# Kernel tuning notes

Hardware: AMD Instinct MI355X
Metric: run time of the kernel (lower is better)

The kernel has to match this reference:

```python
import jax, jax.numpy as jnp
import numpy as np

B, E, C, N, NNZ = 64, 100000, 80000, 10000, 1600000
EPS = 1e-5  # GroupLayerNorm eps


def setup_inputs() -> dict:
    key = jax.random.key(0)
    ks = jax.random.split(key, 8)
    x = jax.random.normal(ks[0], (B, E), dtype=jnp.float32)
    # sparse layer nonzero coordinates (graph-structure-constrained weights)
    w_in_rows = jax.random.randint(ks[1], (NNZ,), 0, E)    # edge index (input dim)
    w_in_cols = jax.random.randint(ks[2], (NNZ,), 0, C)    # hidden channel index
    w_out_rows = jax.random.randint(ks[3], (NNZ,), 0, C)   # hidden channel index
    w_out_cols = jax.random.randint(ks[4], (NNZ,), 0, E)   # edge index (output dim)
    # xavier-like scale: avg fan_in per hidden channel ~ NNZ/C
    scale_in = np.sqrt(2.0 / (NNZ / C + NNZ / E)).astype(np.float32)
    v_in = jax.random.normal(ks[5], (NNZ,), dtype=jnp.float32) * scale_in
    v_out = jax.random.normal(ks[6], (NNZ,), dtype=jnp.float32) * scale_in
    b_in = jnp.zeros((C,), jnp.float32)
    b_out = jnp.zeros((E,), jnp.float32)
    gamma = jnp.ones((C,), jnp.float32)   # GroupLayerNorm affine scale (per channel)
    beta = jnp.zeros((C,), jnp.float32)   # GroupLayerNorm affine shift
    channel_groups = jnp.arange(C, dtype=jnp.int64) // (C // N)  # 8 channels per node
    return {
        'x': x, 'v_in': v_in, 'b_in': b_in, 'v_out': v_out, 'b_out': b_out,
        'gamma': gamma, 'beta': beta,
        'w_in_rows': w_in_rows, 'w_in_cols': w_in_cols,
        'w_out_rows': w_out_rows, 'w_out_cols': w_out_cols,
        'channel_groups': channel_groups,
    }


def _sparse_linear(x, rows, cols, values, bias, out_dim):
    # out[b, c] = sum_{k: cols[k]==c} x[b, rows[k]] * values[k] + bias[c]
    contrib = x[:, rows] * values  # [B, nnz]
    out = jnp.zeros((x.shape[0], out_dim), x.dtype).at[:, cols].add(contrib)
    return out + bias


def _group_layer_norm(h, groups, gamma, beta):
    # per-node-group layernorm over that node's channels
    Bsz = h.shape[0]
    counts = jnp.zeros((N,), h.dtype).at[groups].add(1.0)
    gsum = jnp.zeros((Bsz, N), h.dtype).at[:, groups].add(h)
    gsq = jnp.zeros((Bsz, N), h.dtype).at[:, groups].add(h * h)
    mean = gsum / counts
    var = gsq / counts - mean * mean
    hn = (h - mean[:, groups]) * jax.lax.rsqrt(var[:, groups] + EPS)
    return gamma * hn + beta


def reference(x, v_in, b_in, v_out, b_out, gamma, beta,
              w_in_rows, w_in_cols, w_out_rows, w_out_cols, channel_groups):
    # 1. input sparse linear: edges -> hidden channels
    h = _sparse_linear(x, w_in_rows, w_in_cols, v_in, b_in, C)
    # 2. norm_first=True: GroupLayerNorm then nonlinearity (ELU)
    h = _group_layer_norm(h, channel_groups, gamma, beta)
    h = jax.nn.elu(h)
    # 3. output sparse linear: hidden channels -> edges
    out = _sparse_linear(h, w_out_rows, w_out_cols, v_out, b_out, E)
    # 4. dropout p=0 (identity), residual
    return out + x
```

## Files before the change

### kernel.cpp

```cpp
#include <hip/hip_runtime.h>
#include <hip/hip_bf16.h>

#define B_   64
#define E_   100000
#define C_   80000
#define N_   10000
#define GS   8
#define NNZ_ 1600000
#define EPS_ 1e-5f

#define SHIFT 7
#define BK    128
#define NBLK  256
#define CHUNK (NNZ_ / NBLK)
#define NBMAX 800
#define SCAN_CHUNK 1024
#define SORTT 512
#define PT    1024
#define NTT   782
#define BSCAP 3072

__global__ __launch_bounds__(SORTT) void prep_kernel(
        const float* __restrict__ x, __hip_bfloat16* __restrict__ xT,
        const int* __restrict__ cols1, int* __restrict__ blkcnt1, int nb1,
        const int* __restrict__ cols2, int* __restrict__ blkcnt2, int nb2) {
    __shared__ int hist[NBMAX];
    __shared__ float tile[2][64][65];
    const int b = blockIdx.x;
    const int t = threadIdx.x;
    if (b < 2 * NBLK) {
        const bool p2 = b >= NBLK;
        const int* __restrict__ cols = p2 ? cols2 : cols1;
        int* __restrict__ blkcnt     = p2 ? blkcnt2 : blkcnt1;
        const int nb  = p2 ? nb2 : nb1;
        const int blk = p2 ? (b - NBLK) : b;
        for (int j = t; j < nb; j += SORTT) hist[j] = 0;
        __syncthreads();
        const int base = blk * CHUNK;
        const int end  = min(NNZ_, base + CHUNK);
        for (int k = base + t; k < end; k += SORTT)
            atomicAdd(&hist[cols[k] >> SHIFT], 1);
        __syncthreads();
        for (int j = t; j < nb; j += SORTT) blkcnt[j * NBLK + blk] = hist[j];
    } else {
        const int tb  = b - 2 * NBLK;
        const int sub = t >> 8;
        const int tt  = t & 255;
        const int c   = tt & 63;
        const int r4  = tt >> 6;
        const int e0  = tb * 128 + sub * 64;
#pragma unroll
        for (int j = 0; j < 16; ++j) {
            int br = r4 * 16 + j;
            int e  = e0 + c;
            if (e < E_) tile[sub][c][br] = x[br * E_ + e];
        }
        __syncthreads();
#pragma unroll
        for (int j = 0; j < 16; ++j) {
            int er = r4 * 16 + j;
            int e  = e0 + er;
            if (e < E_) xT[e * 64 + c] = __float2bfloat16(tile[sub][er][c]);
        }
    }
}

__global__ void scan_partial_kernel(const int* __restrict__ c1, int* __restrict__ p1,
                                    int dim1, int np1,
                                    const int* __restrict__ c2, int* __restrict__ p2,
                                    int dim2) {
    __shared__ int red[256];
    const bool ph2 = (int)blockIdx.x >= np1;
    const int* __restrict__ counts = ph2 ? c2 : c1;
    int* __restrict__ partials     = ph2 ? p2 : p1;
    const int dim = ph2 ? dim2 : dim1;
    const int cb  = ph2 ? (blockIdx.x - np1) : blockIdx.x;
    const int t    = threadIdx.x;
    const int base = cb * SCAN_CHUNK + t * 4;
    int s = 0;
#pragma unroll
    for (int j = 0; j < 4; ++j) { int i = base + j; if (i < dim) s += counts[i]; }
    red[t] = s;
    __syncthreads();
    for (int d = 128; d > 0; d >>= 1) {
        if (t < d) red[t] += red[t + d];
        __syncthreads();
    }
    if (t == 0) partials[cb] = red[0];
}

__global__ void scan_base_kernel(int* __restrict__ p1, int np1,
                                 int* __restrict__ p2, int np2) {
    __shared__ int buf[256];
    int* __restrict__ partials = blockIdx.x ? p2 : p1;
    const int nparts           = blockIdx.x ? np2 : np1;
    const int t = threadIdx.x;
    buf[t] = (t < nparts) ? partials[t] : 0;
    __syncthreads();
    for (int d = 1; d < 256; d <<= 1) {
        int v = (t >= d) ? buf[t - d] : 0;
        __syncthreads();
        buf[t] += v;
        __syncthreads();
    }
    if (t < nparts) partials[t] = (t == 0) ? 0 : buf[t - 1];
}

__global__ void scan_emit_kernel(const int* __restrict__ c1, const int* __restrict__ p1,
                                 int* __restrict__ b1, int dim1, int np1,
                                 const int* __restrict__ c2, const int* __restrict__ p2,
                                 int* __restrict__ b2, int dim2) {
    __shared__ int red[256];
    const bool ph2 = (int)blockIdx.x >= np1;
    const int* __restrict__ counts   = ph2 ? c2 : c1;
    const int* __restrict__ partials = ph2 ? p2 : p1;
    int* __restrict__ bases          = ph2 ? b2 : b1;
    const int dim = ph2 ? dim2 : dim1;
    const int cb  = ph2 ? (blockIdx.x - np1) : blockIdx.x;
    const int t    = threadIdx.x;
    const int base = cb * SCAN_CHUNK + t * 4;
    int v[4];
    int s = 0;
#pragma unroll
    for (int j = 0; j < 4; ++j) {
        int i = base + j;
        v[j] = (i < dim) ? counts[i] : 0;
        s += v[j];
    }
    red[t] = s;
    __syncthreads();
    for (int d = 1; d < 256; d <<= 1) {
        int u = (t >= d) ? red[t - d] : 0;
        __syncthreads();
        red[t] += u;
        __syncthreads();
    }
    int run = partials[cb] + ((t == 0) ? 0 : red[t - 1]);
#pragma unroll
    for (int j = 0; j < 4; ++j) {
        int i = base + j;
        if (i < dim) bases[i] = run;
        run += v[j];
    }
}

__global__ __launch_bounds__(PT) void place_kernel(const int* __restrict__ rows,
                             const int* __restrict__ cols,
                             const float* __restrict__ vals, const int* __restrict__ bases,
                             uint2* __restrict__ binned, int nb) {
    __shared__ uint2 staged[CHUNK];
    __shared__ unsigned short bof[CHUNK];
    __shared__ int hist[NBMAX];
    __shared__ int cur[NBMAX];
    __shared__ int goff[NBMAX];
    __shared__ int red[PT];
    const int t    = threadIdx.x;
    const int blk  = blockIdx.x;
    const int base = blk * CHUNK;
    const int n    = min(NNZ_, base + CHUNK) - base;
    for (int j = t; j < nb; j += PT) hist[j] = 0;
    __syncthreads();
    for (int k = t; k < n; k += PT) atomicAdd(&hist[cols[base + k] >> SHIFT], 1);
    __syncthreads();
    int lv[2];
    int s = 0;
    const int b0 = t * 2;
#pragma unroll
    for (int j = 0; j < 2; ++j) {
        int idx = b0 + j;
        lv[j] = (idx < nb) ? hist[idx] : 0;
        s += lv[j];
    }
    red[t] = s;
    __syncthreads();
    for (int d = 1; d < PT; d <<= 1) {
        int v = (t >= d) ? red[t - d] : 0;
        __syncthreads();
        red[t] += v;
        __syncthreads();
    }
    int run = (t == 0) ? 0 : red[t - 1];
#pragma unroll
    for (int j = 0; j < 2; ++j) {
        int idx = b0 + j;
        if (idx < nb) {
            cur[idx]  = run;
            goff[idx] = bases[idx * NBLK + blk] - run;
        }
        run += lv[j];
    }
    __syncthreads();
    for (int k = t; k < n; k += PT) {
        const int c = cols[base + k];
        const int j = c >> SHIFT;
        const int p = atomicAdd(&cur[j], 1);
        staged[p] = make_uint2((unsigned)rows[base + k] | ((unsigned)(c & (BK - 1)) << 17),
                               __float_as_uint(vals[base + k]));
        bof[p] = (unsigned short)j;
    }
    __syncthreads();
    for (int k = t; k < n; k += PT) {
        const int j = bof[k];
        binned[goff[j] + k] = staged[k];
    }
}

__global__ __launch_bounds__(PT) void binsort_kernel(const uint2* __restrict__ binned,
                               const int* __restrict__ bases,
                               int* __restrict__ offsets, float2* __restrict__ csr,
                               int nb, int dim) {
    __shared__ int hist[BK];
    __shared__ int sc[BK];
    __shared__ int cur[BK];
    __shared__ float2 stage[BSCAP];
    const int t   = threadIdx.x;
    const int bkt = blockIdx.x;
    if (t < BK) hist[t] = 0;
    __syncthreads();
    const int beg = bases[bkt * NBLK];
    const int end = (bkt + 1 < nb) ? bases[(bkt + 1) * NBLK] : NNZ_;
    const int cnt = end - beg;
    for (int i = beg + t; i < end; i += PT)
        atomicAdd(&hist[binned[i].x >> 17], 1);
    __syncthreads();
    if (t < BK) sc[t] = hist[t];
    __syncthreads();
    for (int d = 1; d < BK; d <<= 1) {
        int v = (t < BK && t >= d) ? sc[t - d] : 0;
        __syncthreads();
        if (t < BK) sc[t] += v;
        __syncthreads();
    }
    const bool inlds = (cnt <= BSCAP);
    if (t < BK) {
        const int exl = (t == 0) ? 0 : sc[t - 1];
        cur[t] = inlds ? exl : beg + exl;
        const int c = bkt * BK + t;
        if (c < dim) offsets[c] = beg + exl;
    }
    if (t == 0 && bkt == nb - 1) offsets[dim] = NNZ_;
    __syncthreads();
    if (inlds) {
        for (int i = beg + t; i < end; i += PT) {
            const uint2 e = binned[i];
            const int pos = atomicAdd(&cur[e.x >> 17], 1);
            stage[pos] = make_float2(__int_as_float((int)(e.x & 0x1FFFFu)),
                                     __uint_as_float(e.y));
        }
        __syncthreads();
        for (int k = t; k < cnt; k += PT) csr[beg + k] = stage[k];
    } else {
        for (int i = beg + t; i < end; i += PT) {
            const uint2 e = binned[i];
            const int pos = atomicAdd(&cur[e.x >> 17], 1);
            csr[pos] = make_float2(__int_as_float((int)(e.x & 0x1FFFFu)),
                                   __uint_as_float(e.y));
        }
    }
}

__device__ __forceinline__ float col_dot(const float2* __restrict__ csr,
                                         const __hip_bfloat16* __restrict__ src,
                                         int beg, int end, int lane, float a0i) {
    float a[16];
    a[0] = a0i;
#pragma unroll
    for (int j = 1; j < 16; ++j) a[j] = 0.f;
    const __hip_bfloat16* __restrict__ srcl = src + lane;
    int i = beg;
#define USTEP(J)                                                                \
    {                                                                           \
        const float2 eJ = csr[i + (J)];                                         \
        const int    rJ = __float_as_int(eJ.x);                                 \
        a[J] = fmaf(eJ.y, __bfloat162float(srcl[rJ * 64]), a[J]);               \
    }
    for (; i + 16 <= end; i += 16) {
        USTEP(0)  USTEP(1)  USTEP(2)  USTEP(3)
        USTEP(4)  USTEP(5)  USTEP(6)  USTEP(7)
        USTEP(8)  USTEP(9)  USTEP(10) USTEP(11)
        USTEP(12) USTEP(13) USTEP(14) USTEP(15)
    }
    for (; i + 4 <= end; i += 4) {
        USTEP(0) USTEP(1) USTEP(2) USTEP(3)
    }
    for (; i < end; ++i) {
        USTEP(0)
    }
#undef USTEP
    const float s01 = (a[0] + a[1]) + (a[2] + a[3]);
    const float s23 = (a[4] + a[5]) + (a[6] + a[7]);
    const float s45 = (a[8] + a[9]) + (a[10] + a[11]);
    const float s67 = (a[12] + a[13]) + (a[14] + a[15]);
    return (s01 + s23) + (s45 + s67);
}

__global__ __launch_bounds__(256, 8) void gather_kernel(
        const float2* __restrict__ csr, const int* __restrict__ offsets,
        const __hip_bfloat16* __restrict__ src, const float* __restrict__ bias,
        __hip_bfloat16* __restrict__ dst, int dim) {
    const int wave = (blockIdx.x * blockDim.x + threadIdx.x) >> 6;
    const int lane = threadIdx.x & 63;
    if (wave >= dim) return;
    const int beg = __builtin_amdgcn_readfirstlane(offsets[wave]);
    const int end = __builtin_amdgcn_readfirstlane(offsets[wave + 1]);
    dst[wave * 64 + lane] = __float2bfloat16(
        col_dot(csr, src, beg, end, lane, bias ? bias[wave] : 0.f));
}

__global__ void gln_elu_kernel(__hip_bfloat16* __restrict__ h,
                               const float* __restrict__ gamma, const float* __restrict__ beta) {
    const int wave = (blockIdx.x * blockDim.x + threadIdx.x) >> 6;
    const int b    = threadIdx.x & 63;
    if (wave >= N_) return;
    const int c0 = wave * GS;
    float v[GS];
    float s = 0.f, s2 = 0.f;
#pragma unroll
    for (int j = 0; j < GS; ++j) {
        float t = __bfloat162float(h[(c0 + j) * 64 + b]);
        v[j] = t;
        s  += t;
        s2 += t * t;
    }
    const float mean = s * (1.0f / GS);
    const float var  = s2 * (1.0f / GS) - mean * mean;
    const float inv  = rsqrtf(var + EPS_);
#pragma unroll
    for (int j = 0; j < GS; ++j) {
        float hn = (v[j] - mean) * inv;
        float g  = gamma[c0 + j] * hn + beta[c0 + j];
        h[(c0 + j) * 64 + b] = __float2bfloat16((g > 0.f) ? g : expm1f(g));
    }
}

__global__ void finalize_kernel(const __hip_bfloat16* __restrict__ outT,
                                const float* __restrict__ x,
                                const float* __restrict__ b_out, float* __restrict__ out) {
    __shared__ float tile[64][65];
    const int e0 = blockIdx.x * 64;
    const int t  = threadIdx.x;
    const int c  = t & 63;
    const int r4 = t >> 6;
#pragma unroll
    for (int j = 0; j < 16; ++j) {
        int er = r4 * 16 + j;
        int e  = e0 + er;
        if (e < E_) tile[er][c] = __bfloat162float(outT[e * 64 + c]);
    }
    __syncthreads();
#pragma unroll
    for (int j = 0; j < 16; ++j) {
        int br = r4 * 16 + j;
        int e  = e0 + c;
        if (e < E_) out[br * E_ + e] = tile[c][br] + b_out[e] + x[br * E_ + e];
    }
}

extern "C" void kernel_launch(void* const* d_in, const int* in_sizes, int n_in,
                              void* d_out, int out_size, void* d_ws, size_t ws_size,
                              hipStream_t stream) {
    const float* x     = (const float*)d_in[0];
    const float* v_in  = (const float*)d_in[1];
    const float* b_in  = (const float*)d_in[2];
    const float* v_out = (const float*)d_in[3];
    const float* b_out = (const float*)d_in[4];
    const float* gamma = (const float*)d_in[5];
    const float* beta  = (const float*)d_in[6];
    const int* w_in_rows  = (const int*)d_in[7];
    const int* w_in_cols  = (const int*)d_in[8];
    const int* w_out_rows = (const int*)d_in[9];
    const int* w_out_cols = (const int*)d_in[10];
    float* out = (float*)d_out;

    const int nb_C  = (C_ + BK - 1) >> SHIFT;
    const int nb_E  = (E_ + BK - 1) >> SHIFT;
    const int dim_C = nb_C * NBLK;
    const int dim_E = nb_E * NBLK;
    const int np_C  = (dim_C + SCAN_CHUNK - 1) / SCAN_CHUNK;
    const int np_E  = (dim_E + SCAN_CHUNK - 1) / SCAN_CHUNK;

    __hip_bfloat16* xT = (__hip_bfloat16*)d_ws;
    __hip_bfloat16* h  = xT + (size_t)E_ * 64;
    int*    blkcnt1  = (int*)(h + (size_t)C_ * 64);
    int*    blkcnt2  = blkcnt1 + dim_C;
    int*    bases1   = blkcnt2 + dim_E;
    int*    bases2   = bases1 + dim_C;
    int*    partials1 = bases2 + dim_E;
    int*    partials2 = partials1 + 256;
    int*    offsets  = partials2 + 256;
    uint2*  binned   = (uint2*)(offsets + 100002);
    float2* csr      = (float2*)(binned + NNZ_);

    prep_kernel<<<2 * NBLK + NTT, SORTT, 0, stream>>>(
        x, xT, w_in_cols, blkcnt1, nb_C, w_out_cols, blkcnt2, nb_E);
    scan_partial_kernel<<<np_C + np_E, 256, 0, stream>>>(
        blkcnt1, partials1, dim_C, np_C, blkcnt2, partials2, dim_E);
    scan_base_kernel<<<2, 256, 0, stream>>>(partials1, np_C, partials2, np_E);
    scan_emit_kernel<<<np_C + np_E, 256, 0, stream>>>(
        blkcnt1, partials1, bases1, dim_C, np_C, blkcnt2, partials2, bases2, dim_E);

    place_kernel<<<NBLK, PT, 0, stream>>>(w_in_rows, w_in_cols, v_in, bases1, binned, nb_C);
    binsort_kernel<<<nb_C, PT, 0, stream>>>(binned, bases1, offsets, csr, nb_C, C_);
    gather_kernel<<<(C_ + 3) / 4, 256, 0, stream>>>(csr, offsets, xT, b_in, h, C_);
    gln_elu_kernel<<<(N_ + 3) / 4, 256, 0, stream>>>(h, gamma, beta);

    place_kernel<<<NBLK, PT, 0, stream>>>(w_out_rows, w_out_cols, v_out, bases2, binned, nb_E);
    binsort_kernel<<<nb_E, PT, 0, stream>>>(binned, bases2, offsets, csr, nb_E, E_);
    gather_kernel<<<(E_ + 3) / 4, 256, 0, stream>>>(csr, offsets, h, nullptr, xT, E_);

    finalize_kernel<<<(E_ + 63) / 64, 256, 0, stream>>>(xT, x, b_out, out);
}
```

Measured before the change: 284.7 us.

## Batch place and binsort for both sparse layers into single launches

```diff
diff --git a/kernel.cpp b/kernel.cpp
--- a/kernel.cpp
+++ b/kernel.cpp
@@ -18,7 +18,7 @@
 #define SORTT 512
 #define PT    1024
 #define NTT   782
-#define BSCAP 3072
+#define BSCAP 4096
 
 __global__ __launch_bounds__(SORTT) void prep_kernel(
         const float* __restrict__ x, __hip_bfloat16* __restrict__ xT,
@@ -144,18 +144,28 @@
     }
 }
 
-__global__ __launch_bounds__(PT) void place_kernel(const int* __restrict__ rows,
-                             const int* __restrict__ cols,
-                             const float* __restrict__ vals, const int* __restrict__ bases,
-                             uint2* __restrict__ binned, int nb) {
+__global__ __launch_bounds__(PT) void place_both_kernel(
+        const int* __restrict__ rows1, const int* __restrict__ cols1,
+        const float* __restrict__ vals1, const int* __restrict__ bases1,
+        uint2* __restrict__ binned1, int nb1,
+        const int* __restrict__ rows2, const int* __restrict__ cols2,
+        const float* __restrict__ vals2, const int* __restrict__ bases2,
+        uint2* __restrict__ binned2, int nb2) {
     __shared__ uint2 staged[CHUNK];
     __shared__ unsigned short bof[CHUNK];
     __shared__ int hist[NBMAX];
     __shared__ int cur[NBMAX];
     __shared__ int goff[NBMAX];
     __shared__ int red[PT];
+    const bool p2 = blockIdx.x >= NBLK;
+    const int* __restrict__ rows   = p2 ? rows2 : rows1;
+    const int* __restrict__ cols   = p2 ? cols2 : cols1;
+    const float* __restrict__ vals = p2 ? vals2 : vals1;
+    const int* __restrict__ bases  = p2 ? bases2 : bases1;
+    uint2* __restrict__ binned     = p2 ? binned2 : binned1;
+    const int nb   = p2 ? nb2 : nb1;
+    const int blk  = p2 ? (blockIdx.x - NBLK) : blockIdx.x;
     const int t    = threadIdx.x;
-    const int blk  = blockIdx.x;
     const int base = blk * CHUNK;
     const int n    = min(NNZ_, base + CHUNK) - base;
     for (int j = t; j < nb; j += PT) hist[j] = 0;
@@ -205,16 +215,24 @@
     }
 }
 
-__global__ __launch_bounds__(PT) void binsort_kernel(const uint2* __restrict__ binned,
-                               const int* __restrict__ bases,
-                               int* __restrict__ offsets, float2* __restrict__ csr,
-                               int nb, int dim) {
+__global__ __launch_bounds__(PT) void binsort_both_kernel(
+        uint2* __restrict__ binned1, const int* __restrict__ bases1,
+        int* __restrict__ offsets1, int nb1, int dim1,
+        uint2* __restrict__ binned2, const int* __restrict__ bases2,
+        int* __restrict__ offsets2, int nb2, int dim2) {
     __shared__ int hist[BK];
     __shared__ int sc[BK];
     __shared__ int cur[BK];
     __shared__ float2 stage[BSCAP];
-    const int t   = threadIdx.x;
-    const int bkt = blockIdx.x;
+    const bool p2 = (int)blockIdx.x >= nb1;
+    uint2* __restrict__ binned    = p2 ? binned2 : binned1;
+    const int* __restrict__ bases = p2 ? bases2 : bases1;
+    int* __restrict__ offsets     = p2 ? offsets2 : offsets1;
+    const int nb  = p2 ? nb2 : nb1;
+    const int dim = p2 ? dim2 : dim1;
+    const int bkt = p2 ? (blockIdx.x - nb1) : blockIdx.x;
+    float2* __restrict__ csr = (float2*)binned;
+    const int t = threadIdx.x;
     if (t < BK) hist[t] = 0;
     __syncthreads();
     const int beg = bases[bkt * NBLK];
@@ -381,15 +399,16 @@
 
     __hip_bfloat16* xT = (__hip_bfloat16*)d_ws;
     __hip_bfloat16* h  = xT + (size_t)E_ * 64;
-    int*    blkcnt1  = (int*)(h + (size_t)C_ * 64);
+    uint2*  binned1  = (uint2*)(h + (size_t)C_ * 64);
+    uint2*  binned2  = binned1 + NNZ_;
+    int*    blkcnt1  = (int*)(binned2 + NNZ_);
     int*    blkcnt2  = blkcnt1 + dim_C;
     int*    bases1   = blkcnt2 + dim_E;
     int*    bases2   = bases1 + dim_C;
     int*    partials1 = bases2 + dim_E;
     int*    partials2 = partials1 + 256;
-    int*    offsets  = partials2 + 256;
-    uint2*  binned   = (uint2*)(offsets + 100002);
-    float2* csr      = (float2*)(binned + NNZ_);
+    int*    offsets1 = partials2 + 256;
+    int*    offsets2 = offsets1 + (C_ + 2);
 
     prep_kernel<<<2 * NBLK + NTT, SORTT, 0, stream>>>(
         x, xT, w_in_cols, blkcnt1, nb_C, w_out_cols, blkcnt2, nb_E);
@@ -399,14 +418,19 @@
     scan_emit_kernel<<<np_C + np_E, 256, 0, stream>>>(
         blkcnt1, partials1, bases1, dim_C, np_C, blkcnt2, partials2, bases2, dim_E);
 
-    place_kernel<<<NBLK, PT, 0, stream>>>(w_in_rows, w_in_cols, v_in, bases1, binned, nb_C);
-    binsort_kernel<<<nb_C, PT, 0, stream>>>(binned, bases1, offsets, csr, nb_C, C_);
-    gather_kernel<<<(C_ + 3) / 4, 256, 0, stream>>>(csr, offsets, xT, b_in, h, C_);
+    place_both_kernel<<<2 * NBLK, PT, 0, stream>>>(
+        w_in_rows, w_in_cols, v_in, bases1, binned1, nb_C,
+        w_out_rows, w_out_cols, v_out, bases2, binned2, nb_E);
+    binsort_both_kernel<<<nb_C + nb_E, PT, 0, stream>>>(
+        binned1, bases1, offsets1, nb_C, C_,
+        binned2, bases2, offsets2, nb_E, E_);
+
+    gather_kernel<<<(C_ + 3) / 4, 256, 0, stream>>>(
+        (const float2*)binned1, offsets1, xT, b_in, h, C_);
     gln_elu_kernel<<<(N_ + 3) / 4, 256, 0, stream>>>(h, gamma, beta);
 
-    place_kernel<<<NBLK, PT, 0, stream>>>(w_out_rows, w_out_cols, v_out, bases2, binned, nb_E);
-    binsort_kernel<<<nb_E, PT, 0, stream>>>(binned, bases2, offsets, csr, nb_E, E_);
-    gather_kernel<<<(E_ + 3) / 4, 256, 0, stream>>>(csr, offsets, h, nullptr, xT, E_);
+    gather_kernel<<<(E_ + 3) / 4, 256, 0, stream>>>(
+        (const float2*)binned2, offsets2, h, nullptr, xT, E_);
 
     finalize_kernel<<<(E_ + 63) / 64, 256, 0, stream>>>(xT, x, b_out, out);
 }
```

Result: faster. 268.2 us (-5.8%).
